# Kernel tuning notes

Hardware: AMD Instinct MI355X
Metric: run time of the kernel (lower is better)

The kernel has to match this reference:

```python
import jax, jax.numpy as jnp
import numpy as np

V, S, D, H = 32000, 1024, 768, 3072
EPS = 1e-5


def pos_encoding(seq_len, dim, dtype=jnp.float32):
    # pe[pos, i] = sin(pos/10000^(i/dim)) if i even else cos(pos/10000^(i/dim))
    pos = jnp.arange(seq_len, dtype=dtype)[:, None]
    i = jnp.arange(dim, dtype=dtype)[None, :]
    ang = pos / jnp.power(jnp.asarray(10000.0, dtype), i / dim)
    even = (jnp.arange(dim) % 2 == 0)[None, :]
    return jnp.where(even, jnp.sin(ang), jnp.cos(ang))


def layernorm2d(x, w, b):
    # normalizes over last two dims (token_size, input_dim), affine params [S, D]
    m = jnp.mean(x, axis=(-2, -1), keepdims=True)
    v = jnp.mean((x - m) ** 2, axis=(-2, -1), keepdims=True)
    return (x - m) / jnp.sqrt(v + EPS) * w + b


def setup_inputs() -> dict:
    key = jax.random.key(0)
    ks = jax.random.split(key, 16)
    sc = 0.02
    emb = jax.random.normal(ks[0], (V, D), jnp.float32) * sc
    emb = emb.at[0].set(0.0)  # padding_idx=0
    inp = {
        "x": jax.random.randint(ks[1], (8, S), 0, V),
        "emb": emb,
        "Wq": jax.random.normal(ks[2], (D, H), jnp.float32) * sc,
        "bq": jnp.zeros((H,), jnp.float32),
        "Wk": jax.random.normal(ks[3], (D, H), jnp.float32) * sc,
        "bk": jnp.zeros((H,), jnp.float32),
        "Wv": jax.random.normal(ks[4], (D, H), jnp.float32) * sc,
        "bv": jnp.zeros((H,), jnp.float32),
        "Wo": jax.random.normal(ks[5], (H, D), jnp.float32) * sc,
        "bo": jnp.zeros((D,), jnp.float32),
        "W1": jax.random.normal(ks[6], (D, H), jnp.float32) * sc,
        "b1": jnp.zeros((H,), jnp.float32),
        "W2": jax.random.normal(ks[7], (H, D), jnp.float32) * sc,
        "b2": jnp.zeros((D,), jnp.float32),
        "ln1_w": jnp.ones((S, D), jnp.float32),
        "ln1_b": jnp.zeros((S, D), jnp.float32),
        "ln2_w": jnp.ones((S, D), jnp.float32),
        "ln2_b": jnp.zeros((S, D), jnp.float32),
    }
    return inp


def reference(x, emb, Wq, bq, Wk, bk, Wv, bv, Wo, bo, W1, b1, W2, b2, ln1_w, ln1_b, ln2_w, ln2_b):
    y = emb[x]                                   # [B, S, D]
    y = y + pos_encoding(y.shape[1], y.shape[2], y.dtype)
    # unscaled self-attention (no 1/sqrt(d) factor, faithful to source)
    q = y @ Wq + bq
    k = y @ Wk + bk
    v = y @ Wv + bv
    attn = jax.nn.softmax(jnp.einsum("bsh,bth->bst", q, k), axis=-1)
    a = jnp.einsum("bst,bth->bsh", attn, v) @ Wo + bo
    y = layernorm2d(y + a, ln1_w, ln1_b)
    # FFN: GELU applied AFTER second linear (faithful to source)
    f = jax.nn.gelu((y @ W1 + b1) @ W2 + b2, approximate=False)
    y = layernorm2d(y + f, ln2_w, ln2_b)
    return y
```

## Files before the change

### kernel.cpp

```cpp
#include <hip/hip_runtime.h>
#include <hip/hip_fp16.h>

#define DI __device__ __forceinline__

typedef _Float16 f16x8 __attribute__((ext_vector_type(8)));
typedef float f32x4 __attribute__((ext_vector_type(4)));

struct alignas(8) h4 { __half x, y, z, w; };

DI float waveReduceSum(float v) {
#pragma unroll
  for (int i = 1; i < 64; i <<= 1) v += __shfl_xor(v, i);
  return v;
}
DI float waveReduceMax(float v) {
#pragma unroll
  for (int i = 1; i < 64; i <<= 1) v = fmaxf(v, __shfl_xor(v, i));
  return v;
}

DI float gelu_exact(float x) { return 0.5f * x * (1.f + erff(x * 0.70710678118654752f)); }

#define MFMA16(b_, a_, c_) __builtin_amdgcn_mfma_f32_16x16x32_f16((b_), (a_), (c_), 0, 0, 0)

template <typename CT, bool BIAS, bool BROW>
__global__ __launch_bounds__(512, 2) void gemm_nt8(
    const __half* __restrict__ A, int lda, long long sA,
    const __half* __restrict__ Bt, int ldb, long long sB,
    const float* __restrict__ bias, long long sBias,
    CT* __restrict__ C, int ldc, long long sC,
    int nT, int K) {
  __shared__ __align__(16) __half As[2][16384];
  __shared__ __align__(16) __half Bs[2][16384];

  const int tid = threadIdx.x;
  const int wave = tid >> 6, lane = tid & 63;

  const int cpx = gridDim.x >> 3;
  const int bid = (blockIdx.x & 7) * cpx + (blockIdx.x >> 3);

  const int gsz = 4 * nT;
  const int g = bid / gsz, r = bid % gsz;
  const int m0 = (g * 4 + (r & 3)) * 256;
  const int n0 = (r >> 2) * 256;

  A += (long long)blockIdx.z * sA;
  Bt += (long long)blockIdx.z * sB;
  C += (long long)blockIdx.z * sC;
  if constexpr (BIAS || BROW) bias += (long long)blockIdx.z * sBias;

  const int wm = wave >> 2, wn = wave & 3;

  f32x4 acc[8][4];
#pragma unroll
  for (int i = 0; i < 8; ++i)
#pragma unroll
    for (int j = 0; j < 4; ++j) acc[i][j] = (f32x4){0.f, 0.f, 0.f, 0.f};

  const int srow = tid >> 3;
  const int gc = (tid & 7) ^ (srow & 7);
  const __half* Ag = A + (size_t)(m0 + srow) * lda + gc * 8;
  const __half* Bg = Bt + (size_t)(n0 + srow) * ldb + gc * 8;
  const size_t a64 = (size_t)64 * lda, b64 = (size_t)64 * ldb;
  char* AsWr = (char*)As + tid * 16;
  char* BsWr = (char*)Bs + tid * 16;

  f16x8 sra[4], srb[4];

#define LDG(t)                                                        \
  {                                                                   \
    const __half* sa_ = Ag + (t) * 64;                                \
    const __half* sb_ = Bg + (t) * 64;                                \
    sra[0] = *(const f16x8*)(sa_);                                    \
    sra[1] = *(const f16x8*)(sa_ + a64);                              \
    sra[2] = *(const f16x8*)(sa_ + 2 * a64);                          \
    sra[3] = *(const f16x8*)(sa_ + 3 * a64);                          \
    srb[0] = *(const f16x8*)(sb_);                                    \
    srb[1] = *(const f16x8*)(sb_ + b64);                              \
    srb[2] = *(const f16x8*)(sb_ + 2 * b64);                          \
    srb[3] = *(const f16x8*)(sb_ + 3 * b64);                          \
  }
#define DSW(t)                                                        \
  {                                                                   \
    char* da_ = AsWr + (((t) & 1) ? 32768 : 0);                       \
    char* db_ = BsWr + (((t) & 1) ? 32768 : 0);                       \
    *(f16x8*)(da_) = sra[0];                                          \
    *(f16x8*)(da_ + 8192) = sra[1];                                   \
    *(f16x8*)(da_ + 16384) = sra[2];                                  \
    *(f16x8*)(da_ + 24576) = sra[3];                                  \
    *(f16x8*)(db_) = srb[0];                                          \
    *(f16x8*)(db_ + 8192) = srb[1];                                   \
    *(f16x8*)(db_ + 16384) = srb[2];                                  \
    *(f16x8*)(db_ + 24576) = srb[3];                                  \
  }

  const int ml = lane & 15, q = lane >> 4, lx = lane & 7;
  const int co0 = (q ^ lx) * 16, co1 = co0 ^ 64;
  const char* Ar = (const char*)As + wm * 16384 + ml * 128;
  const char* Br = (const char*)Bs + (wn >> 1) * 16384 + (wn & 1) * 8192 + ml * 128;

  const int nt = K >> 6;
  LDG(0);
  DSW(0);
  if (nt > 1) LDG(1);
  asm volatile("s_waitcnt lgkmcnt(0)" ::: "memory");
  __builtin_amdgcn_s_barrier();
  __builtin_amdgcn_sched_barrier(0);

  for (int t = 0; t < nt; ++t) {
    if (t + 1 < nt) {
      DSW(t + 1);
      if (t + 2 < nt) LDG(t + 2);
    }
    const int pb = (t & 1) ? 32768 : 0;
    const char* Ap = Ar + pb;
    const char* Bp = Br + pb;
    f16x8 af[8], bf[4];
#pragma unroll
    for (int ks = 0; ks < 2; ++ks) {
      const int co = ks ? co1 : co0;
#pragma unroll
      for (int i = 0; i < 8; ++i) af[i] = *(const f16x8*)(Ap + i * 2048 + co);
#pragma unroll
      for (int j = 0; j < 4; ++j) bf[j] = *(const f16x8*)(Bp + j * 2048 + co);
#pragma unroll
      for (int i = 0; i < 8; ++i)
#pragma unroll
        for (int j = 0; j < 4; ++j)
          acc[i][j] = MFMA16(bf[j], af[i], acc[i][j]);
    }
    asm volatile("s_waitcnt lgkmcnt(0)" ::: "memory");
    __builtin_amdgcn_s_barrier();
    __builtin_amdgcn_sched_barrier(0);
  }
#undef LDG
#undef DSW

#pragma unroll
  for (int j = 0; j < 4; ++j) {
    const int col0 = n0 + wn * 64 + j * 16 + q * 4;
    float4 bc = {0.f, 0.f, 0.f, 0.f};
    if constexpr (BIAS) bc = *(const float4*)(bias + col0);
#pragma unroll
    for (int i = 0; i < 8; ++i) {
      const int row = m0 + wm * 128 + i * 16 + ml;
      const float br = BROW ? bias[row] : 0.f;
      const float v0 = acc[i][j][0] + bc.x + br;
      const float v1 = acc[i][j][1] + bc.y + br;
      const float v2 = acc[i][j][2] + bc.z + br;
      const float v3 = acc[i][j][3] + bc.w + br;
      if constexpr (sizeof(CT) == 4) {
        *(float4*)(C + (size_t)row * ldc + col0) = make_float4(v0, v1, v2, v3);
      } else {
        h4 o{__float2half(v0), __float2half(v1), __float2half(v2), __float2half(v3)};
        *(h4*)((__half*)C + (size_t)row * ldc + col0) = o;
      }
    }
  }
}

template <typename CT, bool BIAS, bool BROW>
__global__ __launch_bounds__(256, 3) void gemm_nt(
    const __half* __restrict__ A, int lda, long long sA,
    const __half* __restrict__ Bt, int ldb, long long sB,
    const float* __restrict__ bias, long long sBias,
    CT* __restrict__ C, int ldc, long long sC,
    int nT, int K) {
  __shared__ __align__(16) __half As[8192];
  __shared__ __align__(16) __half Bs[8192];

  const int tid = threadIdx.x;
  const int wave = tid >> 6, lane = tid & 63;

  const int cpx = gridDim.x >> 3;
  const int bid = (blockIdx.x & 7) * cpx + (blockIdx.x >> 3);

  const int gsz = 8 * nT;
  const int g = bid / gsz, r = bid % gsz;
  const int m0 = (g * 8 + (r & 7)) * 128;
  const int n0 = (r >> 3) * 128;

  A += (long long)blockIdx.z * sA;
  Bt += (long long)blockIdx.z * sB;
  C += (long long)blockIdx.z * sC;
  if constexpr (BIAS || BROW) bias += (long long)blockIdx.z * sBias;
  const int wm = wave & 1, wn = wave >> 1;

  f32x4 acc[4][4];
#pragma unroll
  for (int i = 0; i < 4; ++i)
#pragma unroll
    for (int jj = 0; jj < 4; ++jj) acc[i][jj] = (f32x4){0.f, 0.f, 0.f, 0.f};

  const int srow = tid >> 3;
  const int gc = (tid & 7) ^ (srow & 7);
  const __half* Ag = A + (size_t)(m0 + srow) * lda + gc * 8;
  const __half* Bg = Bt + (size_t)(n0 + srow) * ldb + gc * 8;
  const size_t a32 = (size_t)32 * lda, b32 = (size_t)32 * ldb;
  char* AsWr = (char*)As + tid * 16;
  char* BsWr = (char*)Bs + tid * 16;

  f16x8 sra[4], srb[4];

#define LDG(t)                                                        \
  {                                                                   \
    const __half* sa_ = Ag + (t) * 64;                                \
    const __half* sb_ = Bg + (t) * 64;                                \
    sra[0] = *(const f16x8*)(sa_);                                    \
    sra[1] = *(const f16x8*)(sa_ + a32);                              \
    sra[2] = *(const f16x8*)(sa_ + 2 * a32);                          \
    sra[3] = *(const f16x8*)(sa_ + 3 * a32);                          \
    srb[0] = *(const f16x8*)(sb_);                                    \
    srb[1] = *(const f16x8*)(sb_ + b32);                              \
    srb[2] = *(const f16x8*)(sb_ + 2 * b32);                          \
    srb[3] = *(const f16x8*)(sb_ + 3 * b32);                          \
  }
#define DSW()                                                         \
  {                                                                   \
    *(f16x8*)(AsWr) = sra[0];                                         \
    *(f16x8*)(AsWr + 4096) = sra[1];                                  \
    *(f16x8*)(AsWr + 8192) = sra[2];                                  \
    *(f16x8*)(AsWr + 12288) = sra[3];                                 \
    *(f16x8*)(BsWr) = srb[0];                                         \
    *(f16x8*)(BsWr + 4096) = srb[1];                                  \
    *(f16x8*)(BsWr + 8192) = srb[2];                                  \
    *(f16x8*)(BsWr + 12288) = srb[3];                                 \
  }

  const int ml = lane & 15, q = lane >> 4, lx = lane & 7;
  const int aoff = ((wm * 64 + ml) * 8 + (q ^ lx)) * 16;
  const int boff = ((wn * 64 + ml) * 8 + (q ^ lx)) * 16;

  const int nt = K >> 6;
  LDG(0);
  for (int t = 0; t < nt; ++t) {
    DSW();
    asm volatile("s_waitcnt lgkmcnt(0)" ::: "memory");
    __builtin_amdgcn_s_barrier();
    __builtin_amdgcn_sched_barrier(0);
    if (t + 1 < nt) LDG(t + 1);
#pragma unroll
    for (int jj = 0; jj < 2; ++jj) {
      const char* Ab = (const char*)As + (jj ? (aoff ^ 64) : aoff);
      const char* Bb = (const char*)Bs + (jj ? (boff ^ 64) : boff);
      f16x8 af[4], bf[4];
#pragma unroll
      for (int i = 0; i < 4; ++i) {
        af[i] = *(const f16x8*)(Ab + i * 2048);
        bf[i] = *(const f16x8*)(Bb + i * 2048);
      }
#pragma unroll
      for (int i = 0; i < 4; ++i)
#pragma unroll
        for (int jn = 0; jn < 4; ++jn)
          acc[i][jn] = MFMA16(bf[jn], af[i], acc[i][jn]);
    }
    asm volatile("s_waitcnt lgkmcnt(0)" ::: "memory");
    __builtin_amdgcn_s_barrier();
    __builtin_amdgcn_sched_barrier(0);
  }
#undef LDG
#undef DSW

#pragma unroll
  for (int jn = 0; jn < 4; ++jn) {
    const int col0 = n0 + wn * 64 + jn * 16 + q * 4;
    float4 bc = {0.f, 0.f, 0.f, 0.f};
    if constexpr (BIAS) bc = *(const float4*)(bias + col0);
#pragma unroll
    for (int i = 0; i < 4; ++i) {
      const int row = m0 + wm * 64 + i * 16 + ml;
      const float br = BROW ? bias[row] : 0.f;
      const float v0 = acc[i][jn][0] + bc.x + br;
      const float v1 = acc[i][jn][1] + bc.y + br;
      const float v2 = acc[i][jn][2] + bc.z + br;
      const float v3 = acc[i][jn][3] + bc.w + br;
      if constexpr (sizeof(CT) == 4) {
        *(float4*)(C + (size_t)row * ldc + col0) = make_float4(v0, v1, v2, v3);
      } else {
        h4 o{__float2half(v0), __float2half(v1), __float2half(v2), __float2half(v3)};
        *(h4*)((__half*)C + (size_t)row * ldc + col0) = o;
      }
    }
  }
}

__global__ __launch_bounds__(256) void prep(
    const float* __restrict__ Wq, const float* __restrict__ Wk,
    const float* __restrict__ Wv, const float* __restrict__ W1,
    const float* __restrict__ Wo, const float* __restrict__ W2,
    const float* __restrict__ bq, const float* __restrict__ bk,
    __half* __restrict__ wD, __half* __restrict__ wB, __half* __restrict__ wC,
    __half* __restrict__ wA, float* __restrict__ bqk) {
  if (blockIdx.x == 2304) {
    if (blockIdx.y == 0)
      for (int i = threadIdx.x; i < 3072; i += 256) {
        bqk[i] = bq[i];
        bqk[3072 + i] = bk[i];
      }
    return;
  }
  __shared__ float t[32][33];
  const int tx = threadIdx.x & 31, ty = threadIdx.x >> 5;
  if (blockIdx.y < 4) {
    const float* in;
    __half* out;
    switch (blockIdx.y) {
      case 0: in = Wq; out = wD; break;
      case 1: in = Wk; out = wD + 3072 * 768; break;
      case 2: in = Wv; out = wB; break;
      default: in = W1; out = wC; break;
    }
    const int cb = blockIdx.x % 96, rb = blockIdx.x / 96;
    const int c = cb * 32 + tx, r0 = rb * 32;
#pragma unroll
    for (int i = 0; i < 32; i += 8) t[ty + i][tx] = in[(size_t)(r0 + ty + i) * 3072 + c];
    __syncthreads();
    const int oc = r0 + tx, o0 = cb * 32;
#pragma unroll
    for (int i = 0; i < 32; i += 8)
      out[(size_t)(o0 + ty + i) * 768 + oc] = __float2half(t[tx][ty + i]);
  } else {
    const float* in = (blockIdx.y == 5) ? W2 : Wo;
    __half* out = wA + ((blockIdx.y == 5) ? 3072 * 768 : 0);
    const int cb = blockIdx.x % 24, rb = blockIdx.x / 24;
    const int c = cb * 32 + tx, r0 = rb * 32;
#pragma unroll
    for (int i = 0; i < 32; i += 8) t[ty + i][tx] = in[(size_t)(r0 + ty + i) * 768 + c];
    __syncthreads();
    const int oc = r0 + tx, o0 = cb * 32;
#pragma unroll
    for (int i = 0; i < 32; i += 8)
      out[(size_t)(o0 + ty + i) * 3072 + oc] = __float2half(t[tx][ty + i]);
  }
}

__global__ __launch_bounds__(256) void embed_pos_kernel(
    const int* __restrict__ x, const float* __restrict__ emb,
    float* __restrict__ y, __half* __restrict__ yh) {
  const int row = blockIdx.x;
  const int s = row & 1023;
  const int tok = x[row];
  const float* ep = emb + (size_t)tok * 768;
  float* yp = y + (size_t)row * 768;
  __half* hp = yh + (size_t)row * 768;
  const float c = -13.287712379549449f / 768.f;
  for (int d = threadIdx.x; d < 768; d += 256) {
    float ang = (float)s * exp2f((float)d * c);
    float pe = (d & 1) ? cosf(ang) : sinf(ang);
    float v = ep[d] + pe;
    yp[d] = v;
    hp[d] = __float2half(v);
  }
}

__global__ __launch_bounds__(256) void softmax_rows(
    const float* __restrict__ L, __half* __restrict__ P) {
  const size_t row = blockIdx.x;
  const float4 x = ((const float4*)(L + row * 1024))[threadIdx.x];
  const int wave = threadIdx.x >> 6, lane = threadIdx.x & 63;
  float m = fmaxf(fmaxf(x.x, x.y), fmaxf(x.z, x.w));
  m = waveReduceMax(m);
  __shared__ float sm[4];
  __shared__ float ssum[4];
  if (lane == 0) sm[wave] = m;
  __syncthreads();
  m = fmaxf(fmaxf(sm[0], sm[1]), fmaxf(sm[2], sm[3]));
  float e0 = expf(x.x - m), e1 = expf(x.y - m), e2 = expf(x.z - m), e3 = expf(x.w - m);
  float s = e0 + e1 + e2 + e3;
  s = waveReduceSum(s);
  if (lane == 0) ssum[wave] = s;
  __syncthreads();
  s = ssum[0] + ssum[1] + ssum[2] + ssum[3];
  const float inv = 1.f / s;
  h4 o{__float2half(e0 * inv), __float2half(e1 * inv), __float2half(e2 * inv),
       __float2half(e3 * inv)};
  ((h4*)(P + row * 1024))[threadIdx.x] = o;
}

template <bool GELU>
__global__ __launch_bounds__(256) void residual_stats(
    float* __restrict__ y, const float* __restrict__ p0, const float* __restrict__ p1,
    const float* __restrict__ bias, float2* __restrict__ partials) {
  const int b = blockIdx.y, chunk = blockIdx.x;
  const size_t base = (size_t)b * 786432 + (size_t)chunk * 8192;
  float4* yp = (float4*)(y + base);
  const float4* a0 = (const float4*)(p0 + base);
  const float4* a1 = (const float4*)(p1 + base);
  float s = 0.f, ss = 0.f;
#pragma unroll
  for (int it = 0; it < 8; ++it) {
    const int idx = it * 256 + threadIdx.x;
    const int d = (chunk * 8192 + it * 1024 + threadIdx.x * 4) % 768;
    float4 yv = yp[idx];
    float4 v0 = a0[idx];
    float4 v1 = a1[idx];
    const float4 bv = *(const float4*)(bias + d);
    float ax = v0.x + v1.x + bv.x, ay = v0.y + v1.y + bv.y;
    float az = v0.z + v1.z + bv.z, aw = v0.w + v1.w + bv.w;
    if constexpr (GELU) {
      ax = gelu_exact(ax); ay = gelu_exact(ay);
      az = gelu_exact(az); aw = gelu_exact(aw);
    }
    float4 r{yv.x + ax, yv.y + ay, yv.z + az, yv.w + aw};
    yp[idx] = r;
    s += r.x + r.y + r.z + r.w;
    ss += r.x * r.x + r.y * r.y + r.z * r.z + r.w * r.w;
  }
  s = waveReduceSum(s);
  ss = waveReduceSum(ss);
  __shared__ float2 wr[4];
  const int wave = threadIdx.x >> 6, lane = threadIdx.x & 63;
  if (lane == 0) wr[wave] = make_float2(s, ss);
  __syncthreads();
  if (threadIdx.x == 0) {
    float S = wr[0].x + wr[1].x + wr[2].x + wr[3].x;
    float SS = wr[0].y + wr[1].y + wr[2].y + wr[3].y;
    partials[b * 96 + chunk] = make_float2(S, SS);
  }
}

template <bool WB>
__global__ __launch_bounds__(256) void ln_apply(
    float* __restrict__ y, __half* __restrict__ yh, const float* __restrict__ w,
    const float* __restrict__ bb, const float2* __restrict__ partials) {
  const unsigned i4 = blockIdx.x * 256 + threadIdx.x;
  const unsigned i = i4 * 4;
  const unsigned b = i / 786432u;
  const int tid = threadIdx.x;
  float s = 0.f, ss = 0.f;
  if (tid < 96) {
    float2 p = partials[b * 96 + tid];
    s = p.x;
    ss = p.y;
  }
  s = waveReduceSum(s);
  ss = waveReduceSum(ss);
  __shared__ float2 wsum[4];
  if ((tid & 63) == 0) wsum[tid >> 6] = make_float2(s, ss);
  __syncthreads();
  const float S = wsum[0].x + wsum[1].x + wsum[2].x + wsum[3].x;
  const float SS = wsum[0].y + wsum[1].y + wsum[2].y + wsum[3].y;
  const float inv = 1.f / 786432.f;
  const float mean = S * inv;
  const float rstd = rsqrtf(SS * inv - mean * mean + 1e-5f);

  const unsigned e4 = (i - b * 786432u) >> 2;
  float4 yv = ((const float4*)y)[i4];
  const float4 wv = ((const float4*)w)[e4];
  const float4 bv = ((const float4*)bb)[e4];
  float4 r;
  r.x = (yv.x - mean) * rstd * wv.x + bv.x;
  r.y = (yv.y - mean) * rstd * wv.y + bv.y;
  r.z = (yv.z - mean) * rstd * wv.z + bv.z;
  r.w = (yv.w - mean) * rstd * wv.w + bv.w;
  ((float4*)y)[i4] = r;
  if constexpr (WB) {
    h4 o{__float2half(r.x), __float2half(r.y), __float2half(r.z), __float2half(r.w)};
    ((h4*)yh)[i4] = o;
  }
}

extern "C" void kernel_launch(void* const* d_in, const int* in_sizes, int n_in,
                              void* d_out, int out_size, void* d_ws, size_t ws_size,
                              hipStream_t stream) {
  const int* x = (const int*)d_in[0];
  const float* emb = (const float*)d_in[1];
  const float* Wq = (const float*)d_in[2];
  const float* bq = (const float*)d_in[3];
  const float* Wk = (const float*)d_in[4];
  const float* bk = (const float*)d_in[5];
  const float* Wv = (const float*)d_in[6];
  const float* bv = (const float*)d_in[7];
  const float* Wo = (const float*)d_in[8];
  const float* bo = (const float*)d_in[9];
  const float* W1 = (const float*)d_in[10];
  const float* b1 = (const float*)d_in[11];
  const float* W2 = (const float*)d_in[12];
  const float* b2 = (const float*)d_in[13];
  const float* ln1w = (const float*)d_in[14];
  const float* ln1b = (const float*)d_in[15];
  const float* ln2w = (const float*)d_in[16];
  const float* ln2b = (const float*)d_in[17];

  float* y = (float*)d_out;

  char* ws = (char*)d_ws;
  __half* yh = (__half*)(ws + 0);
  __half* qb = (__half*)(ws + 12582912);
  __half* kb = (__half*)(ws + 62914560);
  __half* Ph = kb;
  __half* vT = (__half*)(ws + 113246208);
  float* abuf = (float*)vT;
  float* Lg = (float*)(ws + 163577856);
  __half* wA = (__half*)(ws + 197132288);
  __half* wD = (__half*)(ws + 206569472);
  __half* wB = (__half*)(ws + 216006656);
  __half* wC = (__half*)(ws + 220725248);
  float* bqk = (float*)(ws + 225443840);
  float2* part = (float2*)(ws + 225468416);
  const size_t WS_NEEDED = 225474624;
  if (ws_size < WS_NEEDED) return;

  const dim3 blk(256), blk8(512);
  const long long SH = 1024LL * 3072, SS = 1024LL * 1024;
  const long long HALF = 25165824;
  float* p1 = abuf + 6291456;

  prep<<<dim3(2305, 6), blk, 0, stream>>>(Wq, Wk, Wv, W1, Wo, W2, bq, bk, wD, wB, wC, wA, bqk);
  embed_pos_kernel<<<dim3(8192), blk, 0, stream>>>(x, emb, y, yh);

  gemm_nt8<__half, true, false><<<dim3(384, 1, 2), blk8, 0, stream>>>(
      yh, 768, 0, wD, 768, 3072LL * 768, bqk, 3072, qb, 3072, HALF, 12, 768);

  gemm_nt<__half, false, true><<<dim3(192, 1, 8), blk, 0, stream>>>(
      wB, 768, 0, yh, 768, 1024LL * 768, bv, 0, vT, 1024, SH, 8, 768);

  gemm_nt<float, false, false><<<dim3(64, 1, 8), blk, 0, stream>>>(
      qb, 3072, SH, kb, 3072, SH, nullptr, 0, Lg, 1024, SS, 8, 3072);

  softmax_rows<<<dim3(8192), blk, 0, stream>>>(Lg, Ph);

  gemm_nt<__half, false, false><<<dim3(192, 1, 8), blk, 0, stream>>>(
      Ph, 1024, SS, vT, 1024, SH, nullptr, 0, (__half*)qb, 3072, SH, 24, 1024);

  gemm_nt<float, false, false><<<dim3(384, 1, 2), blk, 0, stream>>>(
      (__half*)qb, 3072, 1536, wA, 3072, 1536, nullptr, 0, abuf, 768, 6291456, 6, 1536);

  residual_stats<false><<<dim3(96, 8), blk, 0, stream>>>(y, abuf, p1, bo, part);
  ln_apply<true><<<dim3(6144), blk, 0, stream>>>(y, yh, ln1w, ln1b, part);

  gemm_nt<__half, true, false><<<dim3(1536, 1, 1), blk, 0, stream>>>(
      yh, 768, 0, wC, 768, 0, b1, 0, (__half*)qb, 3072, 0, 24, 768);
  gemm_nt<float, false, false><<<dim3(384, 1, 2), blk, 0, stream>>>(
      (__half*)qb, 3072, 1536, wA + 3072 * 768, 3072, 1536, nullptr, 0, abuf, 768, 6291456, 6, 1536);

  residual_stats<true><<<dim3(96, 8), blk, 0, stream>>>(y, abuf, p1, b2, part);
  ln_apply<false><<<dim3(6144), blk, 0, stream>>>(y, nullptr, ln2w, ln2b, part);
}
```

Measured before the change: 741.5 us.

## Fuse output projections with residual add, GELU and LayerNorm partial stats

Replaces the split-K (two-way) Wo and W2 GEMMs plus the separate residual_stats kernel with one GEMM kernel. Its epilogue adds bias, optionally applies GELU, adds into the residual y, and emits per-tile sum and sum-of-squares partials for LayerNorm. This drops the fp32 intermediate buffers and two extra kernel launches. In exchange each GEMM now runs the full K=3072 in 384 blocks without the split-K parallelism, and ln_apply is changed to read 48 partials per batch instead of 96.

```diff
diff --git a/kernel.cpp b/kernel.cpp
--- a/kernel.cpp
+++ b/kernel.cpp
@@ -282,6 +282,138 @@
         *(h4*)((__half*)C + (size_t)row * ldc + col0) = o;
       }
     }
+  }
+}
+
+template <bool GELU>
+__global__ __launch_bounds__(256, 3) void gemm_nt_res(
+    const __half* __restrict__ A, int lda,
+    const __half* __restrict__ Bt, int ldb,
+    const float* __restrict__ bias, float* __restrict__ y,
+    float2* __restrict__ part, int nT, int K) {
+  __shared__ __align__(16) __half As[8192];
+  __shared__ __align__(16) __half Bs[8192];
+
+  const int tid = threadIdx.x;
+  const int wave = tid >> 6, lane = tid & 63;
+
+  const int cpx = gridDim.x >> 3;
+  const int bid = (blockIdx.x & 7) * cpx + (blockIdx.x >> 3);
+
+  const int gsz = 8 * nT;
+  const int g = bid / gsz, r = bid % gsz;
+  const int m0 = (g * 8 + (r & 7)) * 128;
+  const int n0 = (r >> 3) * 128;
+  const int wm = wave & 1, wn = wave >> 1;
+
+  f32x4 acc[4][4];
+#pragma unroll
+  for (int i = 0; i < 4; ++i)
+#pragma unroll
+    for (int jj = 0; jj < 4; ++jj) acc[i][jj] = (f32x4){0.f, 0.f, 0.f, 0.f};
+
+  const int srow = tid >> 3;
+  const int gc = (tid & 7) ^ (srow & 7);
+  const __half* Ag = A + (size_t)(m0 + srow) * lda + gc * 8;
+  const __half* Bg = Bt + (size_t)(n0 + srow) * ldb + gc * 8;
+  const size_t a32 = (size_t)32 * lda, b32 = (size_t)32 * ldb;
+  char* AsWr = (char*)As + tid * 16;
+  char* BsWr = (char*)Bs + tid * 16;
+
+  f16x8 sra[4], srb[4];
+
+#define LDG(t)                                                        \
+  {                                                                   \
+    const __half* sa_ = Ag + (t) * 64;                                \
+    const __half* sb_ = Bg + (t) * 64;                                \
+    sra[0] = *(const f16x8*)(sa_);                                    \
+    sra[1] = *(const f16x8*)(sa_ + a32);                              \
+    sra[2] = *(const f16x8*)(sa_ + 2 * a32);                          \
+    sra[3] = *(const f16x8*)(sa_ + 3 * a32);                          \
+    srb[0] = *(const f16x8*)(sb_);                                    \
+    srb[1] = *(const f16x8*)(sb_ + b32);                              \
+    srb[2] = *(const f16x8*)(sb_ + 2 * b32);                          \
+    srb[3] = *(const f16x8*)(sb_ + 3 * b32);                          \
+  }
+#define DSW()                                                         \
+  {                                                                   \
+    *(f16x8*)(AsWr) = sra[0];                                         \
+    *(f16x8*)(AsWr + 4096) = sra[1];                                  \
+    *(f16x8*)(AsWr + 8192) = sra[2];                                  \
+    *(f16x8*)(AsWr + 12288) = sra[3];                                 \
+    *(f16x8*)(BsWr) = srb[0];                                         \
+    *(f16x8*)(BsWr + 4096) = srb[1];                                  \
+    *(f16x8*)(BsWr + 8192) = srb[2];                                  \
+    *(f16x8*)(BsWr + 12288) = srb[3];                                 \
+  }
+
+  const int ml = lane & 15, q = lane >> 4, lx = lane & 7;
+  const int aoff = ((wm * 64 + ml) * 8 + (q ^ lx)) * 16;
+  const int boff = ((wn * 64 + ml) * 8 + (q ^ lx)) * 16;
+
+  const int nt = K >> 6;
+  LDG(0);
+  for (int t = 0; t < nt; ++t) {
+    DSW();
+    asm volatile("s_waitcnt lgkmcnt(0)" ::: "memory");
+    __builtin_amdgcn_s_barrier();
+    __builtin_amdgcn_sched_barrier(0);
+    if (t + 1 < nt) LDG(t + 1);
+#pragma unroll
+    for (int jj = 0; jj < 2; ++jj) {
+      const char* Ab = (const char*)As + (jj ? (aoff ^ 64) : aoff);
+      const char* Bb = (const char*)Bs + (jj ? (boff ^ 64) : boff);
+      f16x8 af[4], bf[4];
+#pragma unroll
+      for (int i = 0; i < 4; ++i) {
+        af[i] = *(const f16x8*)(Ab + i * 2048);
+        bf[i] = *(const f16x8*)(Bb + i * 2048);
+      }
+#pragma unroll
+      for (int i = 0; i < 4; ++i)
+#pragma unroll
+        for (int jn = 0; jn < 4; ++jn)
+          acc[i][jn] = MFMA16(bf[jn], af[i], acc[i][jn]);
+    }
+    asm volatile("s_waitcnt lgkmcnt(0)" ::: "memory");
+    __builtin_amdgcn_s_barrier();
+    __builtin_amdgcn_sched_barrier(0);
+  }
+#undef LDG
+#undef DSW
+
+  float s = 0.f, ss = 0.f;
+#pragma unroll
+  for (int jn = 0; jn < 4; ++jn) {
+    const int col0 = n0 + wn * 64 + jn * 16 + q * 4;
+    const float4 bc = *(const float4*)(bias + col0);
+#pragma unroll
+    for (int i = 0; i < 4; ++i) {
+      const int row = m0 + wm * 64 + i * 16 + ml;
+      float* yp = y + (size_t)row * 768 + col0;
+      const float4 yv = *(const float4*)yp;
+      float a0 = acc[i][jn][0] + bc.x, a1 = acc[i][jn][1] + bc.y;
+      float a2 = acc[i][jn][2] + bc.z, a3 = acc[i][jn][3] + bc.w;
+      if constexpr (GELU) {
+        a0 = gelu_exact(a0); a1 = gelu_exact(a1);
+        a2 = gelu_exact(a2); a3 = gelu_exact(a3);
+      }
+      const float v0 = yv.x + a0, v1 = yv.y + a1, v2 = yv.z + a2, v3 = yv.w + a3;
+      *(float4*)yp = make_float4(v0, v1, v2, v3);
+      s += v0 + v1 + v2 + v3;
+      ss += v0 * v0 + v1 * v1 + v2 * v2 + v3 * v3;
+    }
+  }
+  s = waveReduceSum(s);
+  ss = waveReduceSum(ss);
+  __shared__ float2 wr[4];
+  if (lane == 0) wr[wave] = make_float2(s, ss);
+  __syncthreads();
+  if (tid == 0) {
+    const float S = wr[0].x + wr[1].x + wr[2].x + wr[3].x;
+    const float SS = wr[0].y + wr[1].y + wr[2].y + wr[3].y;
+    const int idx = (m0 >> 10) * 48 + ((m0 >> 7) & 7) * 6 + (n0 >> 7);
+    part[idx] = make_float2(S, SS);
   }
 }
 
@@ -378,48 +510,6 @@
   ((h4*)(P + row * 1024))[threadIdx.x] = o;
 }
 
-template <bool GELU>
-__global__ __launch_bounds__(256) void residual_stats(
-    float* __restrict__ y, const float* __restrict__ p0, const float* __restrict__ p1,
-    const float* __restrict__ bias, float2* __restrict__ partials) {
-  const int b = blockIdx.y, chunk = blockIdx.x;
-  const size_t base = (size_t)b * 786432 + (size_t)chunk * 8192;
-  float4* yp = (float4*)(y + base);
-  const float4* a0 = (const float4*)(p0 + base);
-  const float4* a1 = (const float4*)(p1 + base);
-  float s = 0.f, ss = 0.f;
-#pragma unroll
-  for (int it = 0; it < 8; ++it) {
-    const int idx = it * 256 + threadIdx.x;
-    const int d = (chunk * 8192 + it * 1024 + threadIdx.x * 4) % 768;
-    float4 yv = yp[idx];
-    float4 v0 = a0[idx];
-    float4 v1 = a1[idx];
-    const float4 bv = *(const float4*)(bias + d);
-    float ax = v0.x + v1.x + bv.x, ay = v0.y + v1.y + bv.y;
-    float az = v0.z + v1.z + bv.z, aw = v0.w + v1.w + bv.w;
-    if constexpr (GELU) {
-      ax = gelu_exact(ax); ay = gelu_exact(ay);
-      az = gelu_exact(az); aw = gelu_exact(aw);
-    }
-    float4 r{yv.x + ax, yv.y + ay, yv.z + az, yv.w + aw};
-    yp[idx] = r;
-    s += r.x + r.y + r.z + r.w;
-    ss += r.x * r.x + r.y * r.y + r.z * r.z + r.w * r.w;
-  }
-  s = waveReduceSum(s);
-  ss = waveReduceSum(ss);
-  __shared__ float2 wr[4];
-  const int wave = threadIdx.x >> 6, lane = threadIdx.x & 63;
-  if (lane == 0) wr[wave] = make_float2(s, ss);
-  __syncthreads();
-  if (threadIdx.x == 0) {
-    float S = wr[0].x + wr[1].x + wr[2].x + wr[3].x;
-    float SS = wr[0].y + wr[1].y + wr[2].y + wr[3].y;
-    partials[b * 96 + chunk] = make_float2(S, SS);
-  }
-}
-
 template <bool WB>
 __global__ __launch_bounds__(256) void ln_apply(
     float* __restrict__ y, __half* __restrict__ yh, const float* __restrict__ w,
@@ -429,8 +519,8 @@
   const unsigned b = i / 786432u;
   const int tid = threadIdx.x;
   float s = 0.f, ss = 0.f;
-  if (tid < 96) {
-    float2 p = partials[b * 96 + tid];
+  if (tid < 48) {
+    float2 p = partials[b * 48 + tid];
     s = p.x;
     ss = p.y;
   }
@@ -491,7 +581,6 @@
   __half* kb = (__half*)(ws + 62914560);
   __half* Ph = kb;
   __half* vT = (__half*)(ws + 113246208);
-  float* abuf = (float*)vT;
   float* Lg = (float*)(ws + 163577856);
   __half* wA = (__half*)(ws + 197132288);
   __half* wD = (__half*)(ws + 206569472);
@@ -505,7 +594,6 @@
   const dim3 blk(256), blk8(512);
   const long long SH = 1024LL * 3072, SS = 1024LL * 1024;
   const long long HALF = 25165824;
-  float* p1 = abuf + 6291456;
 
   prep<<<dim3(2305, 6), blk, 0, stream>>>(Wq, Wk, Wv, W1, Wo, W2, bq, bk, wD, wB, wC, wA, bqk);
   embed_pos_kernel<<<dim3(8192), blk, 0, stream>>>(x, emb, y, yh);
@@ -524,17 +612,14 @@
   gemm_nt<__half, false, false><<<dim3(192, 1, 8), blk, 0, stream>>>(
       Ph, 1024, SS, vT, 1024, SH, nullptr, 0, (__half*)qb, 3072, SH, 24, 1024);
 
-  gemm_nt<float, false, false><<<dim3(384, 1, 2), blk, 0, stream>>>(
-      (__half*)qb, 3072, 1536, wA, 3072, 1536, nullptr, 0, abuf, 768, 6291456, 6, 1536);
-
-  residual_stats<false><<<dim3(96, 8), blk, 0, stream>>>(y, abuf, p1, bo, part);
+  gemm_nt_res<false><<<dim3(384), blk, 0, stream>>>(
+      (__half*)qb, 3072, wA, 3072, bo, y, part, 6, 3072);
   ln_apply<true><<<dim3(6144), blk, 0, stream>>>(y, yh, ln1w, ln1b, part);
 
   gemm_nt<__half, true, false><<<dim3(1536, 1, 1), blk, 0, stream>>>(
       yh, 768, 0, wC, 768, 0, b1, 0, (__half*)qb, 3072, 0, 24, 768);
-  gemm_nt<float, false, false><<<dim3(384, 1, 2), blk, 0, stream>>>(
-      (__half*)qb, 3072, 1536, wA + 3072 * 768, 3072, 1536, nullptr, 0, abuf, 768, 6291456, 6, 1536);
-
-  residual_stats<true><<<dim3(96, 8), blk, 0, stream>>>(y, abuf, p1, b2, part);
+
+  gemm_nt_res<true><<<dim3(384), blk, 0, stream>>>(
+      (__half*)qb, 3072, wA + 3072 * 768, 3072, b2, y, part, 6, 3072);
   ln_apply<false><<<dim3(6144), blk, 0, stream>>>(y, nullptr, ln2w, ln2b, part);
 }
```

Result: faster. 706.0 us (-4.8%).
